# Optimization experiments

Hardware: AMD Instinct MI355X
Metric: run time of the kernel (lower is better)

## Reference

```python
import jax, jax.numpy as jnp
import numpy as np

MARGIN = 0.2
NEG_INF = -1e30


def setup_inputs() -> dict:
    key = jax.random.key(0)
    k1, k2 = jax.random.split(key)
    B, D, C = 384, 256, 48
    features = jax.random.normal(k1, (B, D), dtype=jnp.float32)
    labels = jax.random.randint(k2, (B,), 0, C, dtype=jnp.int32)
    return {"features": features, "labels": labels, "epoch": 5}


def reference(features, labels, epoch):
    B = features.shape[0]
    # pairwise euclidean distance, clamped like torch.clamp(min=1e-11)
    diff = features[:, None, :] - features[None, :, :]          # [B,B,D]
    dist = jnp.sqrt(jnp.clip(jnp.sum(diff * diff, axis=-1), 1e-11))  # [B,B]

    idx = jnp.arange(B)
    same = labels[:, None] == labels[None, :]
    pos_mask = same & (idx[None, :] > idx[:, None])             # pairs (i,j), j>i, same label
    neg_mask = ~same

    # Gumbel-max sampling replaces the per-row np.random.choice host loop.
    gumbel = jax.random.gumbel(jax.random.key(42), (B, B, B), dtype=dist.dtype)

    if epoch > 3:
        # semi-hard negatives: pos_dist < d(i,k) < pos_dist + margin, weights 1/d(i,k)
        d_ik = dist[:, None, :]                                 # [B,1,B]
        d_pos = dist[:, :, None]                                # [B,B,1]
        semi = neg_mask[:, None, :] & (d_ik > d_pos) & (d_ik < d_pos + MARGIN)  # [B,B,B]
        logits = jnp.where(semi, -jnp.log(dist)[:, None, :], NEG_INF)  # log(1/d)
        has_neg = jnp.any(semi, axis=-1)                        # [B,B]
    else:
        # uniform random negative per (i,j) pair
        logits = jnp.where(neg_mask[:, None, :], 0.0, NEG_INF)  # [B,1,B]
        has_neg = jnp.broadcast_to(jnp.any(neg_mask, axis=-1)[:, None], (B, B))

    neg_idx = jnp.argmax(logits + gumbel, axis=-1)              # [B,B]
    neg_dist = jnp.take_along_axis(dist, neg_idx, axis=1)       # d(i, sampled_neg)

    valid = pos_mask & has_neg
    # MarginRankingLoss(neg, pos, target=1) = relu(pos - neg + margin)
    per_pair = jax.nn.relu(dist - neg_dist + MARGIN)
    count = jnp.sum(valid)
    total = jnp.sum(jnp.where(valid, per_pair, 0.0))
    return jnp.where(count > 0, total / jnp.maximum(count, 1), 0.0)
```

## Files before the change

kernel.cpp:

```cpp
#include <hip/hip_runtime.h>
#include <hip/hip_bf16.h>
#include <stdint.h>

#define BSZ 384
#define DD  256
#define NBLK 256
#define NDUAL (BSZ - NBLK)
#define NTHR 768
#define NWAVES 12
#define NEG_BIG -3.0e38f
#define DONE_BASE 0xAAAAAAAAu

__device__ __forceinline__ void threefry_0_42(uint32_t c0, uint32_t c1,
                                              uint32_t& o0, uint32_t& o1) {
    const uint32_t k0 = 0u;
    const uint32_t k1 = 42u;
    const uint32_t k2 = 0u ^ 42u ^ 0x1BD11BDAu;
    uint32_t x0 = c0 + k0;
    uint32_t x1 = c1 + k1;
#define TF_RND(R) { x0 += x1; x1 = (x1 << (R)) | (x1 >> (32 - (R))); x1 ^= x0; }
    TF_RND(13) TF_RND(15) TF_RND(26) TF_RND(6)
    x0 += k1; x1 += k2 + 1u;
    TF_RND(17) TF_RND(29) TF_RND(16) TF_RND(24)
    x0 += k2; x1 += k0 + 2u;
    TF_RND(13) TF_RND(15) TF_RND(26) TF_RND(6)
    x0 += k0; x1 += k1 + 3u;
    TF_RND(17) TF_RND(29) TF_RND(16) TF_RND(24)
    x0 += k1; x1 += k2 + 4u;
    TF_RND(13) TF_RND(15) TF_RND(26) TF_RND(6)
    x0 += k2; x1 += k0 + 5u;
#undef TF_RND
    o0 = x0; o1 = x1;
}

__device__ __forceinline__ float gumbel_at(uint32_t idx) {
    uint32_t r0, r1;
    threefry_0_42(0u, idx, r0, r1);
    uint32_t bits = r0 ^ r1;
    uint32_t mant = bits >> 9;
    float f = __uint_as_float(mant | 0x3F800000u) - 1.0f;
    float u = (mant == 0u) ? 1.17549435e-38f : f;
    return -logf(-logf(u));
}

__global__ __launch_bounds__(NTHR, 4) void fused_kernel(const float* __restrict__ F,
                                                        const int* __restrict__ labels,
                                                        const int* __restrict__ epochp,
                                                        float* __restrict__ tot_slot,
                                                        unsigned int* __restrict__ cnt_slot,
                                                        unsigned int* __restrict__ done,
                                                        float* __restrict__ out) {
    __shared__ float    row[2][BSZ];
    __shared__ float    nlg[2][BSZ];
    __shared__ float4   anc[2][DD/4];
    __shared__ int      slab[BSZ];
    __shared__ int      plist[512];
    __shared__ int      npos;
    __shared__ int      is_last;
    __shared__ float    wtot[NWAVES];
    __shared__ unsigned wcnt[NWAVES];

    const int b    = blockIdx.x;
    const int tid  = threadIdx.x;
    const int wave = tid >> 6;
    const int lane = tid & 63;
    const int rl   = lane >> 3;
    const int s    = lane & 7;

    const int  i0   = b;
    const bool dual = (b < NDUAL);
    const int  i1   = NBLK + b;

    const float4* F4 = (const float4*)F;

    if (tid < BSZ) slab[tid] = labels[tid];
    if (tid == 0) npos = 0;
    if (tid < DD / 4)                 anc[0][tid]          = F4[i0 * (DD / 4) + tid];
    else if (dual && tid < 2 * (DD / 4)) anc[1][tid - DD/4] = F4[i1 * (DD / 4) + (tid - DD/4)];
    __syncthreads();

    const int lab0 = slab[i0];
    const int lab1 = dual ? slab[i1] : -1;
    if (tid < BSZ) {
        if (tid > i0 && slab[tid] == lab0)
            plist[atomicAdd(&npos, 1)] = tid;
        if (dual && tid > i1 && slab[tid] == lab1)
            plist[atomicAdd(&npos, 1)] = 512 | tid;
    }
    const int  epoch   = *epochp;
    const bool semisel = (epoch > 3);
    __syncthreads();

    const int np = npos;
    float    t_total = 0.0f;
    unsigned t_count = 0u;

    if (np > 0) {
        if (dual) {
            for (int c = 0; c < 4; ++c) {
                const int k = c * 96 + wave * 8 + rl;
                const float4* fk = F4 + (size_t)k * (DD / 4);
                float a0 = 0.f, a1 = 0.f, a2 = 0.f, a3 = 0.f;
                float b0 = 0.f, b1 = 0.f, b2 = 0.f, b3 = 0.f;
#pragma unroll
                for (int t = 0; t < 8; ++t) {
                    float4 bb = fk[t * 8 + s];
                    float4 f0 = anc[0][t * 8 + s];
                    float4 f1 = anc[1][t * 8 + s];
                    float d0 = f0.x - bb.x;
                    float d1 = f0.y - bb.y;
                    float d2 = f0.z - bb.z;
                    float d3 = f0.w - bb.w;
                    a0 = fmaf(d0, d0, a0);
                    a1 = fmaf(d1, d1, a1);
                    a2 = fmaf(d2, d2, a2);
                    a3 = fmaf(d3, d3, a3);
                    float e0 = f1.x - bb.x;
                    float e1 = f1.y - bb.y;
                    float e2 = f1.z - bb.z;
                    float e3 = f1.w - bb.w;
                    b0 = fmaf(e0, e0, b0);
                    b1 = fmaf(e1, e1, b1);
                    b2 = fmaf(e2, e2, b2);
                    b3 = fmaf(e3, e3, b3);
                }
                float p = (a0 + a1) + (a2 + a3);
                p += __shfl_down(p, 4, 64);
                p += __shfl_down(p, 2, 64);
                p += __shfl_down(p, 1, 64);
                if (s == 0) row[0][k] = sqrtf(fmaxf(p, 1e-11f));
                float q = (b0 + b1) + (b2 + b3);
                q += __shfl_down(q, 4, 64);
                q += __shfl_down(q, 2, 64);
                q += __shfl_down(q, 1, 64);
                if (s == 0) row[1][k] = sqrtf(fmaxf(q, 1e-11f));
            }
        } else {
            for (int c = 0; c < 4; ++c) {
                const int k = c * 96 + wave * 8 + rl;
                const float4* fk = F4 + (size_t)k * (DD / 4);
                float a0 = 0.f, a1 = 0.f, a2 = 0.f, a3 = 0.f;
#pragma unroll
                for (int t = 0; t < 8; ++t) {
                    float4 bb = fk[t * 8 + s];
                    float4 f0 = anc[0][t * 8 + s];
                    float d0 = f0.x - bb.x;
                    float d1 = f0.y - bb.y;
                    float d2 = f0.z - bb.z;
                    float d3 = f0.w - bb.w;
                    a0 = fmaf(d0, d0, a0);
                    a1 = fmaf(d1, d1, a1);
                    a2 = fmaf(d2, d2, a2);
                    a3 = fmaf(d3, d3, a3);
                }
                float p = (a0 + a1) + (a2 + a3);
                p += __shfl_down(p, 4, 64);
                p += __shfl_down(p, 2, 64);
                p += __shfl_down(p, 1, 64);
                if (s == 0) row[0][k] = sqrtf(fmaxf(p, 1e-11f));
            }
        }
        __syncthreads();
        if (tid < BSZ)       nlg[0][tid]       = semisel ? -logf(row[0][tid])       : 0.0f;
        else if (dual)       nlg[1][tid - BSZ] = semisel ? -logf(row[1][tid - BSZ]) : 0.0f;
        __syncthreads();

        for (int p = wave; p < np; p += NWAVES) {
            const int   e     = plist[p];
            const int   a     = e >> 9;
            const int   j     = e & 511;
            const int   ia    = a ? i1 : i0;
            const int   laba  = a ? lab1 : lab0;
            const float d_pos = row[a][j];
            const float hi    = d_pos + 0.2f;
            float v  = NEG_BIG;
            int   kk = 0;
#pragma unroll
            for (int c = 0; c < BSZ / 64; ++c) {
                const int   k   = c * 64 + lane;
                const float dkk = row[a][k];
                const bool cand = (slab[k] != laba) &&
                                  (!semisel || (dkk > d_pos && dkk < hi));
                if (__any(cand)) {
                    if (cand) {
                        const uint32_t idx = (uint32_t)(ia * BSZ + j) * (uint32_t)BSZ
                                             + (uint32_t)k;
                        float val = nlg[a][k] + gumbel_at(idx);
                        if (val > v) { v = val; kk = k; }
                    }
                }
            }
#pragma unroll
            for (int off = 32; off; off >>= 1) {
                float ov = __shfl_down(v, off, 64);
                int   oi = __shfl_down(kk, off, 64);
                if (ov > v || (ov == v && oi < kk)) { v = ov; kk = oi; }
            }
            if (lane == 0 && v > -1.0e38f) {
                t_total += fmaxf(d_pos - row[a][kk] + 0.2f, 0.0f);
                t_count += 1u;
            }
        }
    }

    if (lane == 0) { wtot[wave] = t_total; wcnt[wave] = t_count; }
    __syncthreads();
    if (tid == 0) {
        float    tt = 0.0f;
        unsigned cc = 0u;
#pragma unroll
        for (int q = 0; q < NWAVES; ++q) { tt += wtot[q]; cc += wcnt[q]; }
        atomicExch(&tot_slot[b], tt);
        atomicExch(&cnt_slot[b], cc);
        __threadfence();
        const unsigned prev = atomicAdd(done, 1u);
        is_last = (prev == DONE_BASE + (unsigned)(NBLK - 1)) ? 1 : 0;
    }
    __syncthreads();

    if (is_last) {
        float    t = 0.0f;
        unsigned c = 0u;
        if (tid < NBLK) {
            t = atomicAdd(&tot_slot[tid], 0.0f);
            c = atomicAdd(&cnt_slot[tid], 0u);
        }
#pragma unroll
        for (int off = 32; off; off >>= 1) {
            t += __shfl_down(t, off, 64);
            c += __shfl_down(c, off, 64);
        }
        if (lane == 0) { wtot[wave] = t; wcnt[wave] = c; }
        __syncthreads();
        if (tid == 0) {
            float    tt = 0.0f;
            unsigned cc = 0u;
#pragma unroll
            for (int q = 0; q < NWAVES; ++q) { tt += wtot[q]; cc += wcnt[q]; }
            out[0] = (cc > 0u) ? (tt / (float)cc) : 0.0f;
        }
    }
}

extern "C" void kernel_launch(void* const* d_in, const int* in_sizes, int n_in,
                              void* d_out, int out_size, void* d_ws, size_t ws_size,
                              hipStream_t stream) {
    const float* F      = (const float*)d_in[0];
    const int*   labels = (const int*)d_in[1];
    const int*   epoch  = (const int*)d_in[2];
    float*       out    = (float*)d_out;

    if (ws_size < (2 * NBLK + 1) * sizeof(float)) return;
    float*        tot_slot = (float*)d_ws;
    unsigned int* cnt_slot = (unsigned int*)d_ws + NBLK;
    unsigned int* done     = (unsigned int*)d_ws + 2 * NBLK;

    fused_kernel<<<NBLK, NTHR, 0, stream>>>(F, labels, epoch,
                                            tot_slot, cnt_slot, done, out);
}
```

Baseline: 69.32 us.

## Compact semi-hard candidates per wave before dense Gumbel evaluation

The per-pair negative search used to evaluate threefry Gumbel noise lane-by-lane across six 64-wide chunks, leaving most lanes idle because few candidates exist. It now ballot-compacts the candidate indices into a per-wave shared list and then evaluates the Gumbel only over the compacted list, 64 at a time, with lowest-index tie-breaking. The per-block total and count are also packed into a single 64-bit atomic slot. The change adds 9 KB of shared memory per block, which may reduce occupancy.

```diff
diff --git a/kernel.cpp b/kernel.cpp
--- a/kernel.cpp
+++ b/kernel.cpp
@@ -46,8 +46,7 @@
 __global__ __launch_bounds__(NTHR, 4) void fused_kernel(const float* __restrict__ F,
                                                         const int* __restrict__ labels,
                                                         const int* __restrict__ epochp,
-                                                        float* __restrict__ tot_slot,
-                                                        unsigned int* __restrict__ cnt_slot,
+                                                        unsigned long long* __restrict__ slot,
                                                         unsigned int* __restrict__ done,
                                                         float* __restrict__ out) {
     __shared__ float    row[2][BSZ];
@@ -55,6 +54,7 @@
     __shared__ float4   anc[2][DD/4];
     __shared__ int      slab[BSZ];
     __shared__ int      plist[512];
+    __shared__ short    cidx[NWAVES][BSZ];
     __shared__ int      npos;
     __shared__ int      is_last;
     __shared__ float    wtot[NWAVES];
@@ -73,10 +73,13 @@
 
     const float4* F4 = (const float4*)F;
 
+    const int  epoch   = *epochp;
+    const bool semisel = (epoch > 3);
+
     if (tid < BSZ) slab[tid] = labels[tid];
     if (tid == 0) npos = 0;
-    if (tid < DD / 4)                 anc[0][tid]          = F4[i0 * (DD / 4) + tid];
-    else if (dual && tid < 2 * (DD / 4)) anc[1][tid - DD/4] = F4[i1 * (DD / 4) + (tid - DD/4)];
+    if (tid < DD / 4)                    anc[0][tid]         = F4[i0 * (DD / 4) + tid];
+    else if (dual && tid < 2 * (DD / 4)) anc[1][tid - DD/4]  = F4[i1 * (DD / 4) + (tid - DD/4)];
     __syncthreads();
 
     const int lab0 = slab[i0];
@@ -87,8 +90,6 @@
         if (dual && tid > i1 && slab[tid] == lab1)
             plist[atomicAdd(&npos, 1)] = 512 | tid;
     }
-    const int  epoch   = *epochp;
-    const bool semisel = (epoch > 3);
     __syncthreads();
 
     const int np = npos;
@@ -165,6 +166,7 @@
         else if (dual)       nlg[1][tid - BSZ] = semisel ? -logf(row[1][tid - BSZ]) : 0.0f;
         __syncthreads();
 
+        short* cl = cidx[wave];
         for (int p = wave; p < np; p += NWAVES) {
             const int   e     = plist[p];
             const int   a     = e >> 9;
@@ -173,22 +175,36 @@
             const int   laba  = a ? lab1 : lab0;
             const float d_pos = row[a][j];
             const float hi    = d_pos + 0.2f;
-            float v  = NEG_BIG;
-            int   kk = 0;
+
+            int ncand = 0;
 #pragma unroll
             for (int c = 0; c < BSZ / 64; ++c) {
                 const int   k   = c * 64 + lane;
                 const float dkk = row[a][k];
                 const bool cand = (slab[k] != laba) &&
                                   (!semisel || (dkk > d_pos && dkk < hi));
-                if (__any(cand)) {
-                    if (cand) {
-                        const uint32_t idx = (uint32_t)(ia * BSZ + j) * (uint32_t)BSZ
-                                             + (uint32_t)k;
-                        float val = nlg[a][k] + gumbel_at(idx);
-                        if (val > v) { v = val; kk = k; }
-                    }
-                }
+                const unsigned long long m = __ballot(cand);
+                if (cand) {
+                    const int pos = ncand +
+                        (int)__popcll(m & ((1ull << lane) - 1ull));
+                    cl[pos] = (short)k;
+                }
+                ncand += (int)__popcll(m);
+            }
+
+            float v  = NEG_BIG;
+            int   kk = 0x7FFF;
+            for (int base = 0; base < ncand; base += 64) {
+                const int  t   = base + lane;
+                float val = NEG_BIG;
+                int   k   = 0x7FFF;
+                if (t < ncand) {
+                    k = (int)cl[t];
+                    const uint32_t idx = (uint32_t)(ia * BSZ + j) * (uint32_t)BSZ
+                                         + (uint32_t)k;
+                    val = nlg[a][k] + gumbel_at(idx);
+                }
+                if (val > v || (val == v && k < kk)) { v = val; kk = k; }
             }
 #pragma unroll
             for (int off = 32; off; off >>= 1) {
@@ -210,8 +226,10 @@
         unsigned cc = 0u;
 #pragma unroll
         for (int q = 0; q < NWAVES; ++q) { tt += wtot[q]; cc += wcnt[q]; }
-        atomicExch(&tot_slot[b], tt);
-        atomicExch(&cnt_slot[b], cc);
+        const unsigned long long pk =
+            ((unsigned long long)cc << 32) |
+            (unsigned long long)__float_as_uint(tt);
+        atomicExch(&slot[b], pk);
         __threadfence();
         const unsigned prev = atomicAdd(done, 1u);
         is_last = (prev == DONE_BASE + (unsigned)(NBLK - 1)) ? 1 : 0;
@@ -222,8 +240,9 @@
         float    t = 0.0f;
         unsigned c = 0u;
         if (tid < NBLK) {
-            t = atomicAdd(&tot_slot[tid], 0.0f);
-            c = atomicAdd(&cnt_slot[tid], 0u);
+            const unsigned long long pk = atomicAdd(&slot[tid], 0ull);
+            c = (unsigned)(pk >> 32);
+            t = __uint_as_float((unsigned)pk);
         }
 #pragma unroll
         for (int off = 32; off; off >>= 1) {
@@ -250,11 +269,10 @@
     const int*   epoch  = (const int*)d_in[2];
     float*       out    = (float*)d_out;
 
-    if (ws_size < (2 * NBLK + 1) * sizeof(float)) return;
-    float*        tot_slot = (float*)d_ws;
-    unsigned int* cnt_slot = (unsigned int*)d_ws + NBLK;
-    unsigned int* done     = (unsigned int*)d_ws + 2 * NBLK;
-
-    fused_kernel<<<NBLK, NTHR, 0, stream>>>(F, labels, epoch,
-                                            tot_slot, cnt_slot, done, out);
-}
+    if (ws_size < NBLK * sizeof(unsigned long long) + sizeof(unsigned int)) return;
+    unsigned long long* slot = (unsigned long long*)d_ws;
+    unsigned int*       done = (unsigned int*)((char*)d_ws
+                                   + NBLK * sizeof(unsigned long long));
+
+    fused_kernel<<<NBLK, NTHR, 0, stream>>>(F, labels, epoch, slot, done, out);
+}
```

Result: no change. 68.37 us (-1.4%).
